# Kernel optimization log

Measured on AMD Instinct MI355X. Metric: run time of the kernel, lower is better.

The kernel has to match this reference:

```python
import jax, jax.numpy as jnp
import numpy as np

EPS_LOG = 1e-10
DECAY = 0.99
RESET_THRESHOLD = 2


def setup_inputs() -> dict:
    key = jax.random.key(0)
    ks = jax.random.split(key, 8)
    B, C_in, T = 4, 1024, 2048
    K, D = 8192, 256
    N = B * T
    return {
        "z": jax.random.normal(ks[0], (B, C_in, T), dtype=jnp.float32),
        "u": jax.random.uniform(ks[1], (N, K), dtype=jnp.float32),
        "Wi": jax.random.normal(ks[2], (D, C_in), dtype=jnp.float32) * 0.02,
        "bi": jax.random.normal(ks[3], (D,), dtype=jnp.float32) * 0.02,
        "Wo": jax.random.normal(ks[4], (C_in, D), dtype=jnp.float32) * 0.02,
        "bo": jax.random.normal(ks[5], (C_in,), dtype=jnp.float32) * 0.02,
        "embedding": jax.random.normal(ks[6], (K, D), dtype=jnp.float32),
        "cluster_size": jnp.zeros((K,), dtype=jnp.float32),
    }


def reference(z, u, Wi, bi, Wo, bo, embedding, cluster_size):
    B, _, T = z.shape
    K, D = embedding.shape
    N = B * T

    # inproj: Conv1d with kernel_size=1 == pointwise linear over channel dim
    z_e = jnp.einsum('bit,di->bdt', z, Wi) + bi[None, :, None]  # (B, D, T)
    z_d = z_e.transpose(0, 2, 1).reshape(N, D)                   # (b t) d

    # squared-euclidean distances via norm expansion
    dist = ((z_d ** 2).sum(axis=1, keepdims=True)
            - 2.0 * (z_d @ embedding.T)
            + (embedding ** 2).sum(axis=1))                      # (N, K)

    # gumbel noise (training=True), softmax_temp = 1.0
    gumbel = -jnp.log(-jnp.log(u + EPS_LOG) + EPS_LOG)
    logits = -dist + gumbel
    y_soft = jax.nn.softmax(logits, axis=-1)                     # (N, K)

    z_q_flat = y_soft @ embedding                                # (N, D)

    # kl_div(log(avg+eps), uniform target of shape (N,K), reduction='sum')
    avg_probs = y_soft.mean(axis=0)                              # (K,)
    inv_k = 1.0 / K
    kl_loss = N * jnp.sum(inv_k * (jnp.log(inv_k) - jnp.log(avg_probs + EPS_LOG)))

    indices = jnp.argmax(y_soft, axis=1)                         # (N,) int

    z_q = z_q_flat.reshape(B, T, D).transpose(0, 2, 1)           # (B, D, T)
    vq_loss = jnp.mean((z_e - jax.lax.stop_gradient(z_q)) ** 2)

    # outproj: Conv1d kernel_size=1
    out = jnp.einsum('bdt,od->bot', z_q, Wo) + bo[None, :, None]  # (B, C_in, T)

    # box_result: active_num uses cluster_size BEFORE the EMA update
    active_num = (cluster_size > RESET_THRESHOLD).sum().astype(z.dtype)
    counts = jnp.zeros((K,), z.dtype).at[indices].add(1.0)       # one-hot column sums
    probs = counts / N                                           # == mean(one_hot, axis=0)
    perplexity = jnp.exp(-jnp.sum(probs * jnp.log(probs + EPS_LOG)))
    new_cluster_size = cluster_size * DECAY + counts * (1.0 - DECAY)

    return out, vq_loss, kl_loss, perplexity, active_num, new_cluster_size
```

## Files before the change

kernel.cpp:

```cpp
#include <hip/hip_runtime.h>
#include <hip/hip_fp16.h>


#define NROWS 8192
#define KCL   8192
#define DDIM  256
#define CIN   1024
#define TSEQ  2048
#define EPSL  1e-10f
#define MHAT  (-140.0f)

#define OUT_SC   (4*CIN*TSEQ)

#define ZD_OFF   0
#define ZQ_OFF   (NROWS*DDIM)
#define E2_OFF   (2*NROWS*DDIM)
#define CS_OFF   (E2_OFF + KCL)
#define CNT_OFF  (CS_OFF + KCL)
#define VQ_OFF   (CNT_OFF + KCL)
#define LINV_OFF (VQ_OFF + 4)

#define ZD2W   0
#define ZQ2W   2097152
#define EBW    4194304
#define ETW    5242880
#define WOBW   6291456
#define ZDBW   6422528
#define E2W    7471104
#define C2W    7479296
#define LINVW  7487488
#define CSUMW  7495680
#define CNTW   7503872
#define VQW    7512064
#define PW     7512128
#define ENDW   (PW + 33554432)
#define LSPW   ZQ2W
#define CVW    (ZQ2W + 131072)
#define CIW    (ZQ2W + 393216)

using short8v = __attribute__((ext_vector_type(8))) short;
using short4v = __attribute__((ext_vector_type(4))) short;
using f32x16  = __attribute__((ext_vector_type(16))) float;

__device__ __forceinline__ ushort f2bf(float f) {
  unsigned int x = __float_as_uint(f);
  return (ushort)((x + 0x7FFFu + ((x >> 16) & 1u)) >> 16);
}
__device__ __forceinline__ float bf2f(ushort h) {
  return __uint_as_float(((unsigned int)h) << 16);
}
__device__ __forceinline__ short8v pack8(float4 a, float4 b) {
  short8v v;
  v[0] = (short)f2bf(a.x); v[1] = (short)f2bf(a.y);
  v[2] = (short)f2bf(a.z); v[3] = (short)f2bf(a.w);
  v[4] = (short)f2bf(b.x); v[5] = (short)f2bf(b.y);
  v[6] = (short)f2bf(b.z); v[7] = (short)f2bf(b.w);
  return v;
}
__device__ __forceinline__ void gload16(const void* g, void* l) {
  __builtin_amdgcn_global_load_lds(
      (const __attribute__((address_space(1))) unsigned int*)g,
      (__attribute__((address_space(3))) unsigned int*)l, 16, 0, 0);
}


__global__ __launch_bounds__(256) void e2_kernel(const float* __restrict__ E,
                                                 float* __restrict__ e2) {
  const int tid = threadIdx.x;
  const int k = blockIdx.x * 64 + (tid >> 2);
  const int p = tid & 3;
  const float* row = E + (size_t)k * DDIM + p * 64;
  float s = 0.f;
#pragma unroll
  for (int j = 0; j < 16; ++j) {
    const float4 v = *reinterpret_cast<const float4*>(row + j * 4);
    s += v.x * v.x + v.y * v.y + v.z * v.z + v.w * v.w;
  }
  s += __shfl_xor(s, 1);
  s += __shfl_xor(s, 2);
  if (p == 0) e2[k] = s;
}

__global__ __launch_bounds__(256) void e2c2_kernel(const float* __restrict__ E,
                                                   float* __restrict__ e2,
                                                   float* __restrict__ c2) {
  const int tid = threadIdx.x;
  const int k = blockIdx.x * 64 + (tid >> 2);
  const int p = tid & 3;
  const float* row = E + (size_t)k * DDIM + p * 64;
  float s = 0.f;
#pragma unroll
  for (int j = 0; j < 16; ++j) {
    const float4 v = *reinterpret_cast<const float4*>(row + j * 4);
    s += v.x * v.x + v.y * v.y + v.z * v.z + v.w * v.w;
  }
  s += __shfl_xor(s, 1);
  s += __shfl_xor(s, 2);
  if (p == 0) { e2[k] = s; c2[k] = -s - MHAT; }
}

__global__ __launch_bounds__(256) void cvtwob_kernel(const float* __restrict__ W,
                                                     ushort* __restrict__ Wb) {
  const size_t i = ((size_t)blockIdx.x * 256 + threadIdx.x) * 8;
  const float4 a = *reinterpret_cast<const float4*>(W + i);
  const float4 b = *reinterpret_cast<const float4*>(W + i + 4);
  *reinterpret_cast<short8v*>(Wb + i) = pack8(a, b);
}

__global__ __launch_bounds__(256) void etprep_kernel(const float* __restrict__ E,
                                                     ushort* __restrict__ ET,
                                                     ushort* __restrict__ EB) {
  __shared__ float tb[64 * 68];
  const int t = threadIdx.x;
  const int kb = (blockIdx.x & 127) * 64;
  const int db = (blockIdx.x >> 7) * 64;
#pragma unroll
  for (int it = 0; it < 4; ++it) {
    const int r = (t >> 4) + it * 16;
    const int c = (t & 15) * 4;
    const float4 v = *reinterpret_cast<const float4*>(E + (size_t)(kb + r) * DDIM + db + c);
    tb[r * 68 + c] = v.x; tb[r * 68 + c + 1] = v.y;
    tb[r * 68 + c + 2] = v.z; tb[r * 68 + c + 3] = v.w;
    short4v o;
    o[0] = (short)f2bf(v.x); o[1] = (short)f2bf(v.y);
    o[2] = (short)f2bf(v.z); o[3] = (short)f2bf(v.w);
    *reinterpret_cast<short4v*>(EB + (size_t)(kb + r) * DDIM + db + c) = o;
  }
  __syncthreads();
  const int dl = t >> 2, kg = (t & 3) * 16;
  short8v o0, o1;
#pragma unroll
  for (int j = 0; j < 8; ++j) o0[j] = (short)f2bf(tb[(kg + j) * 68 + dl]);
#pragma unroll
  for (int j = 0; j < 8; ++j) o1[j] = (short)f2bf(tb[(kg + 8 + j) * 68 + dl]);
  ushort* dst = ET + (size_t)(db + dl) * KCL + kb + kg;
  *reinterpret_cast<short8v*>(dst) = o0;
  *reinterpret_cast<short8v*>(dst + 8) = o1;
}

__global__ __launch_bounds__(256) void inproj32_kernel(const float* __restrict__ z,
                                                       const float* __restrict__ Wi,
                                                       const float* __restrict__ bi,
                                                       float* __restrict__ zd) {
  __shared__ float wi_s[32 * 260];
  __shared__ float zc[32 * 32];
  const int tid = threadIdx.x;
  const int nb = blockIdx.x >> 1, cih = blockIdx.x & 1;
  const int n0 = nb * 32;
  const int b = n0 / TSEQ;
  const int t0 = n0 % TSEQ;
  const float* zb = z + (size_t)b * CIN * TSEQ;
  const int ibase = cih * 512;

  const int dg = tid & 63;
  const int d0 = dg * 4;
  const int wv = tid >> 6;
  const int r0 = wv * 8;

  float acc[4][8];
#pragma unroll
  for (int c = 0; c < 4; ++c)
#pragma unroll
    for (int r = 0; r < 8; ++r) acc[c][r] = 0.f;

  for (int i0 = ibase; i0 < ibase + 512; i0 += 32) {
    __syncthreads();
    {
      const int iiq = (tid & 7) * 4;
      const int dt = tid >> 3;
#pragma unroll
      for (int p = 0; p < 8; ++p) {
        const int d = dt + p * 32;
        const float4 w = *reinterpret_cast<const float4*>(Wi + (size_t)d * CIN + i0 + iiq);
        wi_s[(iiq + 0) * 260 + d] = w.x;
        wi_s[(iiq + 1) * 260 + d] = w.y;
        wi_s[(iiq + 2) * 260 + d] = w.z;
        wi_s[(iiq + 3) * 260 + d] = w.w;
      }
      const int rr = tid & 31;
      const int iib = tid >> 5;
#pragma unroll
      for (int p = 0; p < 4; ++p) {
        const int ii = iib + p * 8;
        zc[ii * 32 + rr] = zb[(size_t)(i0 + ii) * TSEQ + t0 + rr];
      }
    }
    __syncthreads();
#pragma unroll
    for (int ii = 0; ii < 32; ++ii) {
      const float4 w = *reinterpret_cast<const float4*>(&wi_s[ii * 260 + d0]);
#pragma unroll
      for (int rq = 0; rq < 2; ++rq) {
        const float4 zv = *reinterpret_cast<const float4*>(&zc[ii * 32 + r0 + rq * 4]);
        const float zz[4] = {zv.x, zv.y, zv.z, zv.w};
#pragma unroll
        for (int q = 0; q < 4; ++q) {
          acc[0][rq * 4 + q] += w.x * zz[q];
          acc[1][rq * 4 + q] += w.y * zz[q];
          acc[2][rq * 4 + q] += w.z * zz[q];
          acc[3][rq * 4 + q] += w.w * zz[q];
        }
      }
    }
  }
  const float4 bv = *reinterpret_cast<const float4*>(bi + d0);
  const float bx = cih ? 0.f : bv.x, by = cih ? 0.f : bv.y;
  const float bz = cih ? 0.f : bv.z, bw = cih ? 0.f : bv.w;
#pragma unroll
  for (int r = 0; r < 8; ++r) {
    float* zr = zd + (size_t)(n0 + r0 + r) * DDIM + d0;
    atomicAdd(zr + 0, acc[0][r] + bx);
    atomicAdd(zr + 1, acc[1][r] + by);
    atomicAdd(zr + 2, acc[2][r] + bz);
    atomicAdd(zr + 3, acc[3][r] + bw);
  }
}

#define FSS(KT, CUR, UC, UN)                                                   \
  {                                                                            \
    const int k0 = kbase + (KT) * 32;                                          \
    __syncthreads();            \
    if ((KT) < 15) {                                                           \
      _Pragma("unroll")                                                        \
      for (int pp = 0; pp < 2; ++pp) {                                         \
        const int q = tid + pp * 512, r = q >> 5, c = q & 31;                  \
        gload16(Eb + (size_t)(k0 + 32 + r) * 256 + (size_t)(c ^ (r & 7)) * 8,  \
                &Es[(1 - (CUR)) * 8192 + q * 8]);                              \
      }                                                                        \
      const float* ubn = ubase + k0 + 32 + 4 * half;                           \
      _Pragma("unroll")                                                        \
      for (int q = 0; q < 4; ++q)                                              \
        UN[q] = *reinterpret_cast<const float4*>(ubn + q * 8);                 \
    }                                                                          \
    const ushort* Ecur = Es + (CUR) * 8192;                                    \
    f32x16 acc;                                                                \
    _Pragma("unroll")                                                          \
    for (int i = 0; i < 16; ++i) acc[i] = 0.f;                                 \
    _Pragma("unroll")                                                          \
    for (int ks = 0; ks < 16; ++ks) {                                          \
      const int cc = (ks * 2 + half) ^ (r31 & 7);                              \
      const short8v Af =                                                       \
          *reinterpret_cast<const short8v*>(Ecur + r31 * 256 + cc * 8);        \
      acc = __builtin_amdgcn_mfma_f32_32x32x16_bf16(Af, ZB[ks], acc, 0, 0, 0); \
    }                                                                          \
    ushort* pdst = P + (size_t)n * KCL + k0 + 4 * half;                        \
    _Pragma("unroll")                                                          \
    for (int q = 0; q < 4; ++q) {                                              \
      const float uu[4] = {UC[q].x, UC[q].y, UC[q].z, UC[q].w};                \
      short4v st;                                                              \
      _Pragma("unroll")                                                        \
      for (int j = 0; j < 4; ++j) {                                            \
        const int reg = q * 4 + j;                                             \
        const int kcl = k0 + q * 8 + 4 * half + j;                             \
        const float ce = c2s[kcl - kbase];                                     \
        const float D = 1e-10f - __logf(uu[j] + 1e-10f);                       \
        const float pe = __fdividef(__expf(fmaf(acc[reg], 2.f, ce)), D);       \
        psum += pe;                                                            \
        const bool cA = pe > b0v, cB = pe > b1v;                               \
        const float nv = cA ? b0v : pe; const int ni = cA ? b0i : kcl;         \
        b1v = cB ? nv : b1v; b1i = cB ? ni : b1i;                              \
        b0v = cA ? pe : b0v; b0i = cA ? kcl : b0i;                             \
        st[j] = (short)f2bf(pe);                                               \
      }                                                                        \
      *reinterpret_cast<short4v*>(pdst + q * 8) = st;                          \
    }                                                                          \
  }

__global__ __launch_bounds__(512, 2) void flashS_kernel(
    const ushort* __restrict__ ZDB, const float* __restrict__ u,
    const ushort* __restrict__ Eb, const float* __restrict__ c2,
    ushort* __restrict__ P, float* __restrict__ lsp,
    float* __restrict__ candv, int* __restrict__ candi) {
  __shared__ ushort Es[2 * 32 * 256];
  __shared__ float c2s[512];
  const int tid = threadIdx.x;
  const int l = tid & 63, w = tid >> 6;
  const int half = l >> 5;
  const int swz = (blockIdx.x & 7) * 64 + (blockIdx.x >> 3);
  const int nb = swz & 31, kq = swz >> 5;
  const int n0 = nb * 256;
  const int kbase = kq * 512;
  const int r31 = l & 31;
  const int n = n0 + w * 32 + r31;

  short8v ZB[16];
  {
    const ushort* zr = ZDB + (size_t)n * DDIM + half * 8;
#pragma unroll
    for (int ks = 0; ks < 16; ++ks)
      ZB[ks] = *reinterpret_cast<const short8v*>(zr + ks * 16);
  }

  const float* ubase = u + ((size_t)n << 13);
  c2s[tid] = c2[kbase + tid];

#pragma unroll
  for (int pp = 0; pp < 2; ++pp) {
    const int q = tid + pp * 512, r = q >> 5, c = q & 31;
    gload16(Eb + (size_t)(kbase + r) * 256 + (size_t)(c ^ (r & 7)) * 8, &Es[q * 8]);
  }
  float4 uA[4], uB[4];
  {
    const float* ub = ubase + kbase + 4 * half;
#pragma unroll
    for (int q = 0; q < 4; ++q)
      uA[q] = *reinterpret_cast<const float4*>(ub + q * 8);
  }

  float psum = 0.f;
  float b0v = -1.f, b1v = -1.f;
  int b0i = 0x7fffffff, b1i = 0x7fffffff;

  for (int kt2 = 0; kt2 < 16; kt2 += 2) {
    FSS(kt2, 0, uA, uB);
    FSS(kt2 + 1, 1, uB, uA);
  }

  psum += __shfl_xor(psum, 32);
  {
    const float ov0 = __shfl_xor(b0v, 32); const int oi0 = __shfl_xor(b0i, 32);
    const float ov1 = __shfl_xor(b1v, 32); const int oi1 = __shfl_xor(b1i, 32);
    {
      const bool cA = (ov0 > b0v) || (ov0 == b0v && oi0 < b0i);
      const bool cB = (ov0 > b1v) || (ov0 == b1v && oi0 < b1i);
      const float nv = cA ? b0v : ov0; const int ni = cA ? b0i : oi0;
      b1v = cB ? nv : b1v; b1i = cB ? ni : b1i;
      b0v = cA ? ov0 : b0v; b0i = cA ? oi0 : b0i;
    }
    {
      const bool cA = (ov1 > b0v) || (ov1 == b0v && oi1 < b0i);
      const bool cB = (ov1 > b1v) || (ov1 == b1v && oi1 < b1i);
      const float nv = cA ? b0v : ov1; const int ni = cA ? b0i : oi1;
      b1v = cB ? nv : b1v; b1i = cB ? ni : b1i;
      b0v = cA ? ov1 : b0v; b0i = cA ? oi1 : b0i;
    }
  }
  if (half == 0) {
    lsp[kq * NROWS + n] = psum;
    candv[(kq * 2 + 0) * NROWS + n] = b0v;
    candi[(kq * 2 + 0) * NROWS + n] = b0i;
    candv[(kq * 2 + 1) * NROWS + n] = b1v;
    candi[(kq * 2 + 1) * NROWS + n] = b1i;
  }
}

__global__ __launch_bounds__(256) void rowfin_kernel(
    const float* __restrict__ lsp, const float* __restrict__ candv,
    const int* __restrict__ candi, const float* __restrict__ zd,
    const float* __restrict__ E, const float* __restrict__ e2,
    const float* __restrict__ u, float* __restrict__ linv,
    float* __restrict__ counts) {
  const int l = threadIdx.x & 63;
  const int w = threadIdx.x >> 6;
  const int n = blockIdx.x * 4 + w;

  float bv[4] = {-1.f, -1.f, -1.f, -1.f};
  int bi[4] = {0x7fffffff, 0x7fffffff, 0x7fffffff, 0x7fffffff};
  if (l < 32) { bv[0] = candv[l * NROWS + n]; bi[0] = candi[l * NROWS + n]; }
#pragma unroll
  for (int mk = 1; mk < 64; mk <<= 1) {
    float ov[4]; int oi[4];
#pragma unroll
    for (int i = 0; i < 4; ++i) { ov[i] = __shfl_xor(bv[i], mk); oi[i] = __shfl_xor(bi[i], mk); }
#pragma unroll
    for (int i = 0; i < 4; ++i) {
      const float f = ov[i]; const int kk = oi[i];
      const bool c0 = (f > bv[0]) || (f == bv[0] && kk < bi[0]);
      const bool c1 = (f > bv[1]) || (f == bv[1] && kk < bi[1]);
      const bool c2 = (f > bv[2]) || (f == bv[2] && kk < bi[2]);
      const bool c3 = (f > bv[3]) || (f == bv[3] && kk < bi[3]);
      const float n3 = c2 ? bv[2] : f; const int i3 = c2 ? bi[2] : kk;
      const float n2 = c1 ? bv[1] : f; const int i2 = c1 ? bi[1] : kk;
      const float n1 = c0 ? bv[0] : f; const int i1 = c0 ? bi[0] : kk;
      bv[3] = c3 ? n3 : bv[3]; bi[3] = c3 ? i3 : bi[3];
      bv[2] = c2 ? n2 : bv[2]; bi[2] = c2 ? i2 : bi[2];
      bv[1] = c1 ? n1 : bv[1]; bi[1] = c1 ? i1 : bi[1];
      bv[0] = c0 ? f : bv[0];  bi[0] = c0 ? kk : bi[0];
    }
  }
  float ls = (l < 16) ? lsp[l * NROWS + n] : 0.f;
#pragma unroll
  for (int mk = 1; mk <= 8; mk <<= 1) ls += __shfl_xor(ls, mk);
  const float4 zv = *reinterpret_cast<const float4*>(zd + (size_t)n * DDIM + l * 4);
  float best = -1e30f; int besti = 0x7fffffff;
#pragma unroll
  for (int c = 0; c < 4; ++c) {
    const int kc = bi[c];
    const float4 ev = *reinterpret_cast<const float4*>(E + (size_t)kc * DDIM + l * 4);
    float d = zv.x * ev.x + zv.y * ev.y + zv.z * ev.z + zv.w * ev.w;
#pragma unroll
    for (int mk = 1; mk < 64; mk <<= 1) d += __shfl_xor(d, mk);
    const float uu = u[(size_t)n * KCL + kc];
    const float D = 1e-10f - __logf(uu + 1e-10f);
    const float g = -__logf(D);
    const float lg = 2.f * d - e2[kc] + g;
    if (lg > best || (lg == best && kc < besti)) { best = lg; besti = kc; }
  }
  if (l == 0) {
    atomicAdd(&counts[besti], 1.f);
    linv[n] = 1.f / ls;
  }
}

__global__ __launch_bounds__(512, 2) void pvS_kernel(
    const ushort* __restrict__ P, const ushort* __restrict__ ET,
    const float* __restrict__ linv, float* __restrict__ parts,
    float* __restrict__ colsum) {
  __shared__ ushort ps[2][64 * 64];
  __shared__ float linv_s[64];
  const int tid = threadIdx.x;
  const int l = tid & 63, w = tid >> 6;
  const int half = l >> 5;
  const int r31 = l & 31;
  const int swz = (blockIdx.x & 7) * 64 + (blockIdx.x >> 3);
  const int nb = swz & 127, ks = swz >> 7;
  const int n0 = nb * 64;
  const int kc0 = ks * 2048;
  const int nw = w & 1, dw = w >> 1;
  const int sr = tid >> 3, sc = tid & 7;

  if (tid < 64) linv_s[tid] = linv[n0 + tid];

  f32x16 acc0, acc1;
#pragma unroll
  for (int i = 0; i < 16; ++i) { acc0[i] = 0.f; acc1[i] = 0.f; }

  gload16(P + (size_t)(n0 + sr) * KCL + kc0 + (size_t)(sc ^ (sr & 7)) * 8,
          &ps[0][tid * 8]);

  for (int t = 0; t < 32; ++t) {
    const int cur = t & 1;
    const int kc = kc0 + t * 64;
    __syncthreads();
    if (t < 31) {
      gload16(P + (size_t)(n0 + sr) * KCL + kc + 64 + (size_t)(sc ^ (sr & 7)) * 8,
              &ps[1 - cur][tid * 8]);
    }
#pragma unroll
    for (int ksn = 0; ksn < 4; ++ksn) {
      const int cc = ksn * 2 + half;
      short8v a, b0, b1;
      {
        const int r = nw * 32 + r31;
        a = *reinterpret_cast<const short8v*>(&ps[cur][r * 64 + ((cc ^ (r & 7))) * 8]);
      }
      {
        const ushort* etb = ET + (size_t)(dw * 64 + r31) * KCL + kc + cc * 8;
        b0 = *reinterpret_cast<const short8v*>(etb);
        b1 = *reinterpret_cast<const short8v*>(etb + (size_t)32 * KCL);
      }
      acc0 = __builtin_amdgcn_mfma_f32_32x32x16_bf16(a, b0, acc0, 0, 0, 0);
      acc1 = __builtin_amdgcn_mfma_f32_32x32x16_bf16(a, b1, acc1, 0, 0, 0);
    }
    {
      const int c = tid >> 3;
      const int rb = tid & 7;
      float csp = 0.f;
#pragma unroll
      for (int r8 = 0; r8 < 8; ++r8) {
        const int r = rb + r8 * 8;
        const int chunk = (c >> 3) ^ (r & 7);
        csp += bf2f(ps[cur][r * 64 + chunk * 8 + (c & 7)]) * linv_s[r];
      }
      csp += __shfl_xor(csp, 1);
      csp += __shfl_xor(csp, 2);
      csp += __shfl_xor(csp, 4);
      if (rb == 0) atomicAdd(&colsum[kc + c], csp);
    }
  }
  float* pbase = parts + (size_t)ks * NROWS * DDIM;
#pragma unroll
  for (int reg = 0; reg < 16; ++reg) {
    const int dr = (reg & 3) + 8 * (reg >> 2) + 4 * half;
    float* zr = pbase + (size_t)(n0 + nw * 32 + dr) * DDIM + dw * 64 + r31;
    zr[0]  = acc0[reg];
    zr[32] = acc1[reg];
  }
}

__global__ __launch_bounds__(256) void zqred_kernel(const float* __restrict__ parts,
                                                    const float* __restrict__ linv,
                                                    const float* __restrict__ zd,
                                                    float* __restrict__ zq,
                                                    float* __restrict__ vqs) {
  const size_t i = ((size_t)blockIdx.x * 256 + threadIdx.x) * 8;
  const int n = (int)(i >> 8);
  const float lv = linv[n];
  float s = 0.f;
#pragma unroll
  for (int j = 0; j < 8; j += 4) {
    float4 p0 = *reinterpret_cast<const float4*>(parts + i + j);
    const float4 p1 = *reinterpret_cast<const float4*>(parts + i + j + (size_t)NROWS * DDIM);
    const float4 p2 = *reinterpret_cast<const float4*>(parts + i + j + (size_t)2 * NROWS * DDIM);
    const float4 p3 = *reinterpret_cast<const float4*>(parts + i + j + (size_t)3 * NROWS * DDIM);
    const float4 a = *reinterpret_cast<const float4*>(zd + i + j);
    float4 o;
    o.x = (p0.x + p1.x + p2.x + p3.x) * lv;
    o.y = (p0.y + p1.y + p2.y + p3.y) * lv;
    o.z = (p0.z + p1.z + p2.z + p3.z) * lv;
    o.w = (p0.w + p1.w + p2.w + p3.w) * lv;
    *reinterpret_cast<float4*>(zq + i + j) = o;
    const float dx = a.x - o.x, dy = a.y - o.y, dz = a.z - o.z, dw = a.w - o.w;
    s += dx * dx + dy * dy + dz * dz + dw * dw;
  }
#pragma unroll
  for (int mk = 1; mk < 64; mk <<= 1) s += __shfl_xor(s, mk);
  if ((threadIdx.x & 63) == 0) atomicAdd(vqs, s);
}

__global__ __launch_bounds__(256) void outproj2_kernel(const float* __restrict__ zq,
                                                       const ushort* __restrict__ Wob,
                                                       const float* __restrict__ bo,
                                                       float* __restrict__ outp) {
  extern __shared__ char smem[];
  ushort* zs = (ushort*)smem;
  ushort* wsld = zs + 64 * 256;
  const int tid = threadIdx.x;
  const int l = tid & 63, w = tid >> 6;
  const int half = l >> 5;
  const int nb = blockIdx.x >> 4, ob = blockIdx.x & 15;
  const int n0 = nb * 64, o0 = ob * 64;
  const int nw = w & 1, ow = w >> 1;
  {
    const int row = tid >> 2, seg = tid & 3;
    const float* zr = zq + (size_t)(n0 + row) * DDIM + seg * 64;
    const ushort* wr = Wob + (size_t)(o0 + row) * DDIM + seg * 64;
#pragma unroll
    for (int g = 0; g < 8; ++g) {
      const float4 a = *reinterpret_cast<const float4*>(zr + g * 8);
      const float4 b = *reinterpret_cast<const float4*>(zr + g * 8 + 4);
      const int c = seg * 8 + g;
      *reinterpret_cast<short8v*>(zs + row * 256 + ((c ^ (row & 7))) * 8) = pack8(a, b);
      const short8v wv = *reinterpret_cast<const short8v*>(wr + g * 8);
      *reinterpret_cast<short8v*>(wsld + row * 256 + ((c ^ (row & 7))) * 8) = wv;
    }
  }
  __syncthreads();
  f32x16 acc;
#pragma unroll
  for (int i = 0; i < 16; ++i) acc[i] = 0.f;
#pragma unroll
  for (int ksn = 0; ksn < 16; ++ksn) {
    const int cc = ksn * 2 + half;
    const int ra = nw * 32 + (l & 31);
    const int rb = ow * 32 + (l & 31);
    const short8v a = *reinterpret_cast<const short8v*>(zs + ra * 256 + ((cc ^ (ra & 7))) * 8);
    const short8v b = *reinterpret_cast<const short8v*>(wsld + rb * 256 + ((cc ^ (rb & 7))) * 8);
    acc = __builtin_amdgcn_mfma_f32_32x32x16_bf16(a, b, acc, 0, 0, 0);
  }
  const int o = o0 + ow * 32 + (l & 31);
  const float bvv = bo[o];
  const int nbase = n0 + nw * 32 + 4 * half;
#pragma unroll
  for (int rq = 0; rq < 4; ++rq) {
    const int n = nbase + rq * 8;
    const int b = n >> 11;
    const int tt = n & 2047;
    float4 ov;
    ov.x = acc[rq * 4 + 0] + bvv;
    ov.y = acc[rq * 4 + 1] + bvv;
    ov.z = acc[rq * 4 + 2] + bvv;
    ov.w = acc[rq * 4 + 3] + bvv;
    *reinterpret_cast<float4*>(outp + ((size_t)b * CIN + o) * TSEQ + tt) = ov;
  }
}

template <bool STORE_LG>
__global__ __launch_bounds__(512) void flash_kernel(
    const float* __restrict__ zd, const float* __restrict__ u,
    const float* __restrict__ E, const float* __restrict__ e2g,
    float* __restrict__ zq, float* __restrict__ colsum,
    float* __restrict__ counts, float* __restrict__ vqsum,
    float* __restrict__ linvg, __half* __restrict__ lgbuf) {
  extern __shared__ float lds[];
  float* zs = lds;
  float* es = zs + 32 * 260;
  float* e2t = es + 64 * 260;
  float* cst = e2t + 64;
  float* red = cst + 64;

  const int tid = threadIdx.x;
  const int lane = tid & 63;
  const int wv = tid >> 6;
  const int r = (lane >> 4) & 3;
  const int kg = lane & 15;
  const int row = wv * 4 + r;
  const int n0 = blockIdx.x * 32;
  const int n = n0 + row;

  {
    const int rr = tid >> 4;
    const int iq = tid & 15;
#pragma unroll
    for (int p = 0; p < 4; ++p) {
      const int i = iq * 16 + p * 4;
      *reinterpret_cast<float4*>(&zs[rr * 260 + i]) =
          *reinterpret_cast<const float4*>(zd + (size_t)(n0 + rr) * DDIM + i);
    }
  }

  float4 accp[4];
#pragma unroll
  for (int s = 0; s < 4; ++s) accp[s] = make_float4(0.f, 0.f, 0.f, 0.f);
  float lsum = 0.f;
  float best = -1e30f;
  int bidx = 0;

  const float* zrow = zs + row * 260;

  for (int t = 0; t < KCL / 64; ++t) {
    const int k0 = t * 64;
    __syncthreads();
    {
      const int iq = tid & 15;
#pragma unroll
      for (int pp = 0; pp < 2; ++pp) {
        const int kk = (tid >> 4) + pp * 32;
#pragma unroll
        for (int p = 0; p < 4; ++p) {
          const int i = iq * 16 + p * 4;
          *reinterpret_cast<float4*>(&es[kk * 260 + i]) =
              *reinterpret_cast<const float4*>(E + (size_t)(k0 + kk) * DDIM + i);
        }
      }
      if (tid < 64) e2t[tid] = e2g[k0 + tid];
    }
    __syncthreads();

    float acc4[4] = {0.f, 0.f, 0.f, 0.f};
#pragma unroll 4
    for (int i = 0; i < DDIM; i += 4) {
      const float4 zv = *reinterpret_cast<const float4*>(zrow + i);
#pragma unroll
      for (int jj = 0; jj < 4; ++jj) {
        const float4 ev = *reinterpret_cast<const float4*>(&es[(kg + jj * 16) * 260 + i]);
        acc4[jj] += zv.x * ev.x + zv.y * ev.y + zv.z * ev.z + zv.w * ev.w;
      }
    }

    float p4[4];
    float tmax = -1e30f;
    int tidx = 0;
#pragma unroll
    for (int jj = 0; jj < 4; ++jj) {
      const int kk = kg + jj * 16;
      const float uu = u[(size_t)n * KCL + k0 + kk];
      const float g = -__logf(-__logf(uu + EPSL) + EPSL);
      const float lt = 2.f * acc4[jj] - e2t[kk] + g - MHAT;
      const float pe = __expf(lt);
      p4[jj] = pe;
      lsum += pe;
      if (lt > tmax) { tmax = lt; tidx = k0 + kk; }
    }
#pragma unroll
    for (int mk = 1; mk <= 8; mk <<= 1) {
      const float ov = __shfl_xor(tmax, mk);
      const int oi = __shfl_xor(tidx, mk);
      if (ov > tmax || (ov == tmax && oi < tidx)) { tmax = ov; tidx = oi; }
    }
    if (tmax > best) { best = tmax; bidx = tidx; }

#pragma unroll
    for (int jj = 0; jj < 4; ++jj) {
#pragma unroll 4
      for (int q = 0; q < 16; ++q) {
        const int kk = jj * 16 + q;
        const float yv = __shfl(p4[jj], (lane & 48) | q);
        const float* erow = &es[kk * 260 + kg * 16];
#pragma unroll
        for (int s = 0; s < 4; ++s) {
          const int c = (s + kg) & 3;
          const float4 ev = *reinterpret_cast<const float4*>(erow + c * 4);
          accp[s].x += yv * ev.x;
          accp[s].y += yv * ev.y;
          accp[s].z += yv * ev.z;
          accp[s].w += yv * ev.w;
        }
      }
    }
  }

#pragma unroll
  for (int mk = 1; mk <= 8; mk <<= 1) lsum += __shfl_xor(lsum, mk);
  const float linv = 1.0f / lsum;

  if (kg == 0) {
    atomicAdd(&counts[bidx], 1.0f);
    linvg[n] = linv;
  }

  float vqp = 0.f;
#pragma unroll
  for (int s = 0; s < 4; ++s) {
    const int c = (s + kg) & 3;
    const int d = kg * 16 + c * 4;
    float4 o;
    o.x = accp[s].x * linv;
    o.y = accp[s].y * linv;
    o.z = accp[s].z * linv;
    o.w = accp[s].w * linv;
    *reinterpret_cast<float4*>(zq + (size_t)n * DDIM + d) = o;
    const float4 zv = *reinterpret_cast<const float4*>(zrow + d);
    const float dx = zv.x - o.x, dy = zv.y - o.y, dz = zv.z - o.z, dw = zv.w - o.w;
    vqp += dx * dx + dy * dy + dz * dz + dw * dw;
  }
#pragma unroll
  for (int mk = 1; mk <= 32; mk <<= 1) vqp += __shfl_xor(vqp, mk);
  if (lane == 0) red[wv] = vqp;
  __syncthreads();
  if (tid == 0) {
    float s = 0.f;
#pragma unroll
    for (int ww = 0; ww < 8; ++ww) s += red[ww];
    atomicAdd(vqsum, s);
  }

  if (!STORE_LG) {
    if (tid < 64) cst[tid] = 0.f;
    for (int t = 0; t < KCL / 64; ++t) {
      const int k0 = t * 64;
      __syncthreads();
      {
        const int iq = tid & 15;
#pragma unroll
        for (int pp = 0; pp < 2; ++pp) {
          const int kk = (tid >> 4) + pp * 32;
#pragma unroll
          for (int p = 0; p < 4; ++p) {
            const int i = iq * 16 + p * 4;
            *reinterpret_cast<float4*>(&es[kk * 260 + i]) =
                *reinterpret_cast<const float4*>(E + (size_t)(k0 + kk) * DDIM + i);
          }
        }
        if (tid < 64) e2t[tid] = e2g[k0 + tid];
      }
      __syncthreads();
      float acc4[4] = {0.f, 0.f, 0.f, 0.f};
#pragma unroll 4
      for (int i = 0; i < DDIM; i += 4) {
        const float4 zv = *reinterpret_cast<const float4*>(zrow + i);
#pragma unroll
        for (int jj = 0; jj < 4; ++jj) {
          const float4 ev = *reinterpret_cast<const float4*>(&es[(kg + jj * 16) * 260 + i]);
          acc4[jj] += zv.x * ev.x + zv.y * ev.y + zv.z * ev.z + zv.w * ev.w;
        }
      }
      float cs4[4];
#pragma unroll
      for (int jj = 0; jj < 4; ++jj) {
        const int kk = kg + jj * 16;
        const float uu = u[(size_t)n * KCL + k0 + kk];
        const float g = -__logf(-__logf(uu + EPSL) + EPSL);
        const float lt = 2.f * acc4[jj] - e2t[kk] + g - MHAT;
        cs4[jj] = __expf(lt) * linv;
      }
#pragma unroll
      for (int mk = 16; mk <= 32; mk <<= 1)
#pragma unroll
        for (int jj = 0; jj < 4; ++jj) cs4[jj] += __shfl_xor(cs4[jj], mk);
      if (lane < 16) {
#pragma unroll
        for (int jj = 0; jj < 4; ++jj) atomicAdd(&cst[kg + jj * 16], cs4[jj]);
      }
      __syncthreads();
      if (tid < 64) {
        atomicAdd(&colsum[k0 + tid], cst[tid]);
        cst[tid] = 0.f;
      }
    }
  }
}

__global__ __launch_bounds__(256) void outproj_kernel(const float* __restrict__ zq,
                                                      const float* __restrict__ Wo,
                                                      const float* __restrict__ bo,
                                                      float* __restrict__ outp) {
  __shared__ float wo_s[32 * 260];
  __shared__ float zc[32 * 68];
  const int tid = threadIdx.x;
  const int n0 = (blockIdx.x >> 2) * 64;
  const int ot = (blockIdx.x & 3) * 256;
  const int b = n0 / TSEQ;
  const int t0 = n0 % TSEQ;

  const int og = tid & 63;
  const int o0 = og * 4;
  const int wv = tid >> 6;
  const int r0 = wv * 16;

  float acc[4][16];
#pragma unroll
  for (int c = 0; c < 4; ++c)
#pragma unroll
    for (int r = 0; r < 16; ++r) acc[c][r] = 0.f;

  for (int dd = 0; dd < DDIM; dd += 32) {
    __syncthreads();
    {
      const int ccq = (tid & 7) * 4;
      const int oq = tid >> 3;
#pragma unroll
      for (int p = 0; p < 8; ++p) {
        const int oo = oq + p * 32;
        const float4 w = *reinterpret_cast<const float4*>(Wo + (size_t)(ot + oo) * DDIM + dd + ccq);
        wo_s[(ccq + 0) * 260 + oo] = w.x;
        wo_s[(ccq + 1) * 260 + oo] = w.y;
        wo_s[(ccq + 2) * 260 + oo] = w.z;
        wo_s[(ccq + 3) * 260 + oo] = w.w;
      }
#pragma unroll
      for (int p = 0; p < 2; ++p) {
        const int rr = oq + p * 32;
        const float4 v = *reinterpret_cast<const float4*>(zq + (size_t)(n0 + rr) * DDIM + dd + ccq);
        zc[(ccq + 0) * 68 + rr] = v.x;
        zc[(ccq + 1) * 68 + rr] = v.y;
        zc[(ccq + 2) * 68 + rr] = v.z;
        zc[(ccq + 3) * 68 + rr] = v.w;
      }
    }
    __syncthreads();
#pragma unroll
    for (int cc = 0; cc < 32; ++cc) {
      const float4 w = *reinterpret_cast<const float4*>(&wo_s[cc * 260 + o0]);
#pragma unroll
      for (int rq = 0; rq < 4; ++rq) {
        const float4 zv = *reinterpret_cast<const float4*>(&zc[cc * 68 + r0 + rq * 4]);
        const float zz[4] = {zv.x, zv.y, zv.z, zv.w};
#pragma unroll
        for (int q = 0; q < 4; ++q) {
          acc[0][rq * 4 + q] += w.x * zz[q];
          acc[1][rq * 4 + q] += w.y * zz[q];
          acc[2][rq * 4 + q] += w.z * zz[q];
          acc[3][rq * 4 + q] += w.w * zz[q];
        }
      }
    }
  }
  const float4 bv = *reinterpret_cast<const float4*>(bo + ot + o0);
  float* ob = outp + (size_t)b * CIN * TSEQ + t0;
  const float bb[4] = {bv.x, bv.y, bv.z, bv.w};
#pragma unroll
  for (int c = 0; c < 4; ++c) {
#pragma unroll
    for (int rq = 0; rq < 4; ++rq) {
      float4 o;
      o.x = acc[c][rq * 4 + 0] + bb[c];
      o.y = acc[c][rq * 4 + 1] + bb[c];
      o.z = acc[c][rq * 4 + 2] + bb[c];
      o.w = acc[c][rq * 4 + 3] + bb[c];
      *reinterpret_cast<float4*>(ob + (size_t)(ot + o0 + c) * TSEQ + r0 + rq * 4) = o;
    }
  }
}

__global__ __launch_bounds__(256) void finalize_kernel(
    const float* __restrict__ colsum, const float* __restrict__ counts,
    const float* __restrict__ vqsum, const float* __restrict__ csin,
    float* __restrict__ outsc, float* __restrict__ ncs) {
  __shared__ float rS[3][4];
  const int tid = threadIdx.x;
  const int lane = tid & 63;
  const int wv = tid >> 6;
  float sLog = 0.f, sH = 0.f, sAct = 0.f;
  for (int k = tid; k < KCL; k += 256) {
    const float avg = colsum[k] * (1.0f / NROWS);
    sLog += __logf(avg + EPSL);
    const float pb = counts[k] * (1.0f / NROWS);
    sH += pb * __logf(pb + EPSL);
    sAct += (csin[k] > 2.0f) ? 1.f : 0.f;
    ncs[k] = csin[k] * 0.99f + counts[k] * 0.01f;
  }
#pragma unroll
  for (int mk = 1; mk <= 32; mk <<= 1) {
    sLog += __shfl_xor(sLog, mk);
    sH += __shfl_xor(sH, mk);
    sAct += __shfl_xor(sAct, mk);
  }
  if (lane == 0) { rS[0][wv] = sLog; rS[1][wv] = sH; rS[2][wv] = sAct; }
  __syncthreads();
  if (tid == 0) {
    float SL = 0.f, SH = 0.f, SA = 0.f;
#pragma unroll
    for (int w = 0; w < 4; ++w) { SL += rS[0][w]; SH += rS[1][w]; SA += rS[2][w]; }
    outsc[0] = vqsum[0] * (1.0f / ((float)NROWS * (float)DDIM));
    outsc[1] = (float)NROWS * __logf(1.0f / (float)KCL) - SL;
    outsc[2] = __expf(-SH);
    outsc[3] = SA;
  }
}

extern "C" void kernel_launch(void* const* d_in, const int* in_sizes, int n_in,
                              void* d_out, int out_size, void* d_ws, size_t ws_size,
                              hipStream_t stream) {
  (void)in_sizes; (void)n_in; (void)out_size;
  const float* z = (const float*)d_in[0];
  const float* u = (const float*)d_in[1];
  const float* Wi = (const float*)d_in[2];
  const float* bi = (const float*)d_in[3];
  const float* Wo = (const float*)d_in[4];
  const float* bo = (const float*)d_in[5];
  const float* E = (const float*)d_in[6];
  const float* csin = (const float*)d_in[7];
  float* outp = (float*)d_out;
  float* ws = (float*)d_ws;

  const size_t needNew = (size_t)ENDW * 4;
  if (ws_size >= needNew) {
    ushort* EB = (ushort*)(ws + EBW);
    ushort* ET = (ushort*)(ws + ETW);
    ushort* WOB = (ushort*)(ws + WOBW);
    ushort* ZDB = (ushort*)(ws + ZDBW);
    ushort* P = (ushort*)(ws + PW);

    hipMemsetAsync((void*)(ws + CSUMW), 0, (size_t)(2 * KCL + 64) * 4, stream);
    hipMemsetAsync((void*)(ws + ZD2W), 0, (size_t)NROWS * DDIM * 4, stream);

    e2c2_kernel<<<KCL / 64, 256, 0, stream>>>(E, ws + E2W, ws + C2W);
    etprep_kernel<<<512, 256, 0, stream>>>(E, ET, EB);
    cvtwob_kernel<<<128, 256, 0, stream>>>(Wo, WOB);
    inproj32_kernel<<<512, 256, 0, stream>>>(z, Wi, bi, ws + ZD2W);
    cvtwob_kernel<<<1024, 256, 0, stream>>>(ws + ZD2W, ZDB);

    flashS_kernel<<<512, 512, 0, stream>>>(ZDB, u, EB, ws + C2W, P,
                                           ws + LSPW, ws + CVW, (int*)(ws + CIW));
    rowfin_kernel<<<NROWS / 4, 256, 0, stream>>>(ws + LSPW, ws + CVW,
                                                 (const int*)(ws + CIW),
                                                 ws + ZD2W, E, ws + E2W, u,
                                                 ws + LINVW, ws + CNTW);
    pvS_kernel<<<512, 512, 0, stream>>>(P, ET, ws + LINVW, outp, ws + CSUMW);
    zqred_kernel<<<1024, 256, 0, stream>>>(outp, ws + LINVW, ws + ZD2W,
                                           ws + ZQ2W, ws + VQW);

    hipFuncSetAttribute(reinterpret_cast<const void*>(&outproj2_kernel),
                        hipFuncAttributeMaxDynamicSharedMemorySize, 65536);
    outproj2_kernel<<<2048, 256, 65536, stream>>>(ws + ZQ2W, WOB, bo, outp);
    finalize_kernel<<<1, 256, 0, stream>>>(ws + CSUMW, ws + CNTW, ws + VQW,
                                           csin, outp + OUT_SC, outp + OUT_SC + 4);
  } else {
    hipMemsetAsync((void*)(ws + CS_OFF), 0, (size_t)(2 * KCL + 1) * sizeof(float), stream);
    hipMemsetAsync((void*)(ws + ZD_OFF), 0, (size_t)NROWS * DDIM * 4, stream);
    e2_kernel<<<KCL / 64, 256, 0, stream>>>(E, ws + E2_OFF);
    inproj32_kernel<<<512, 256, 0, stream>>>(z, Wi, bi, ws + ZD_OFF);
    const int ldsB = (32 * 260 + 64 * 260 + 64 + 64 + 16) * 4;
    hipFuncSetAttribute(reinterpret_cast<const void*>(&flash_kernel<false>),
                        hipFuncAttributeMaxDynamicSharedMemorySize, ldsB);
    flash_kernel<false><<<NROWS / 32, 512, ldsB, stream>>>(
        ws + ZD_OFF, u, E, ws + E2_OFF, ws + ZQ_OFF, ws + CS_OFF, ws + CNT_OFF,
        ws + VQ_OFF, ws + LINV_OFF, (__half*)nullptr);
    outproj_kernel<<<(NROWS / 64) * 4, 256, 0, stream>>>(ws + ZQ_OFF, Wo, bo, outp);
    finalize_kernel<<<1, 256, 0, stream>>>(ws + CS_OFF, ws + CNT_OFF, ws + VQ_OFF,
                                           csin, outp + OUT_SC, outp + OUT_SC + 4);
  }
}
```

Before: 606.9 us.

## Stage P tile stores through LDS and stage ET tiles in LDS for PV GEMM

The score kernel now writes each wave's bf16 probability tile into a padded LDS buffer and then emits coalesced 16-byte row stores to global P, replacing scattered 8-byte stores. The PV kernel drops the double-buffered async P load and instead prefetches both the P tile and the ET tile into registers. It writes them into swizzled LDS each iteration and reads the MFMA operands from LDS rather than directly from global memory. This targets uncoalesced global traffic in both kernels, at the cost of more LDS use, extra LDS round trips and an additional barrier per iteration, which could reduce occupancy or overlap.

```diff
diff --git a/kernel.cpp b/kernel.cpp
--- a/kernel.cpp
+++ b/kernel.cpp
@@ -243,7 +243,7 @@
           *reinterpret_cast<const short8v*>(Ecur + r31 * 256 + cc * 8);        \
       acc = __builtin_amdgcn_mfma_f32_32x32x16_bf16(Af, ZB[ks], acc, 0, 0, 0); \
     }                                                                          \
-    ushort* pdst = P + (size_t)n * KCL + k0 + 4 * half;                        \
+    ushort* psw = Ps + w * 1280 + r31 * 40 + 4 * half;                         \
     _Pragma("unroll")                                                          \
     for (int q = 0; q < 4; ++q) {                                              \
       const float uu[4] = {UC[q].x, UC[q].y, UC[q].z, UC[q].w};                \
@@ -262,16 +262,27 @@
         b0v = cA ? pe : b0v; b0i = cA ? kcl : b0i;                             \
         st[j] = (short)f2bf(pe);                                               \
       }                                                                        \
-      *reinterpret_cast<short4v*>(pdst + q * 8) = st;                          \
+      *reinterpret_cast<short4v*>(psw + q * 8) = st;                           \
     }                                                                          \
-  }
-
-__global__ __launch_bounds__(512, 2) void flashS_kernel(
+    asm volatile("s_waitcnt lgkmcnt(0)" ::: "memory");                         \
+    __builtin_amdgcn_sched_barrier(0);                                         \
+    {                                                                          \
+      const int frow = l >> 1, fpart = l & 1;                                  \
+      const ushort* src = Ps + w * 1280 + frow * 40 + fpart * 16;              \
+      ushort* dst = P + (size_t)(n0 + w * 32 + frow) * KCL + k0 + fpart * 16;  \
+      *reinterpret_cast<short8v*>(dst) = *reinterpret_cast<const short8v*>(src);\
+      *reinterpret_cast<short8v*>(dst + 8) =                                   \
+          *reinterpret_cast<const short8v*>(src + 8);                          \
+    }                                                                          \
+  }
+
+__global__ __launch_bounds__(512, 2) void flashS2_kernel(
     const ushort* __restrict__ ZDB, const float* __restrict__ u,
     const ushort* __restrict__ Eb, const float* __restrict__ c2,
     ushort* __restrict__ P, float* __restrict__ lsp,
     float* __restrict__ candv, int* __restrict__ candi) {
   __shared__ ushort Es[2 * 32 * 256];
+  __shared__ ushort Ps[8 * 32 * 40];
   __shared__ float c2s[512];
   const int tid = threadIdx.x;
   const int l = tid & 63, w = tid >> 6;
@@ -402,11 +413,12 @@
   }
 }
 
-__global__ __launch_bounds__(512, 2) void pvS_kernel(
+__global__ __launch_bounds__(512, 2) void pv2_kernel(
     const ushort* __restrict__ P, const ushort* __restrict__ ET,
     const float* __restrict__ linv, float* __restrict__ parts,
     float* __restrict__ colsum) {
-  __shared__ ushort ps[2][64 * 64];
+  __shared__ ushort ps[64 * 64];
+  __shared__ ushort es[256 * 64];
   __shared__ float linv_s[64];
   const int tid = threadIdx.x;
   const int l = tid & 63, w = tid >> 6;
@@ -417,7 +429,6 @@
   const int n0 = nb * 64;
   const int kc0 = ks * 2048;
   const int nw = w & 1, dw = w >> 1;
-  const int sr = tid >> 3, sc = tid & 7;
 
   if (tid < 64) linv_s[tid] = linv[n0 + tid];
 
@@ -425,30 +436,46 @@
 #pragma unroll
   for (int i = 0; i < 16; ++i) { acc0[i] = 0.f; acc1[i] = 0.f; }
 
-  gload16(P + (size_t)(n0 + sr) * KCL + kc0 + (size_t)(sc ^ (sr & 7)) * 8,
-          &ps[0][tid * 8]);
-
+  short8v rp, re[4];
+  {
+    const int r = tid >> 3, c = tid & 7;
+    rp = *reinterpret_cast<const short8v*>(P + (size_t)(n0 + r) * KCL + kc0 + c * 8);
+#pragma unroll
+    for (int pp = 0; pp < 4; ++pp) {
+      const int q = tid * 4 + pp; const int rr = q >> 3, cc = q & 7;
+      re[pp] = *reinterpret_cast<const short8v*>(ET + (size_t)rr * KCL + kc0 + cc * 8);
+    }
+  }
   for (int t = 0; t < 32; ++t) {
-    const int cur = t & 1;
-    const int kc = kc0 + t * 64;
+    {
+      const int r = tid >> 3, c = tid & 7;
+      *reinterpret_cast<short8v*>(ps + r * 64 + ((c ^ (r & 7))) * 8) = rp;
+    }
+#pragma unroll
+    for (int pp = 0; pp < 4; ++pp) {
+      const int q = tid * 4 + pp; const int rr = q >> 3, cc = q & 7;
+      *reinterpret_cast<short8v*>(es + rr * 64 + ((cc ^ (rr & 7))) * 8) = re[pp];
+    }
     __syncthreads();
     if (t < 31) {
-      gload16(P + (size_t)(n0 + sr) * KCL + kc + 64 + (size_t)(sc ^ (sr & 7)) * 8,
-              &ps[1 - cur][tid * 8]);
+      const int kc = kc0 + (t + 1) * 64;
+      {
+        const int r = tid >> 3, c = tid & 7;
+        rp = *reinterpret_cast<const short8v*>(P + (size_t)(n0 + r) * KCL + kc + c * 8);
+      }
+#pragma unroll
+      for (int pp = 0; pp < 4; ++pp) {
+        const int q = tid * 4 + pp; const int rr = q >> 3, cc = q & 7;
+        re[pp] = *reinterpret_cast<const short8v*>(ET + (size_t)rr * KCL + kc + cc * 8);
+      }
     }
 #pragma unroll
     for (int ksn = 0; ksn < 4; ++ksn) {
       const int cc = ksn * 2 + half;
       short8v a, b0, b1;
-      {
-        const int r = nw * 32 + r31;
-        a = *reinterpret_cast<const short8v*>(&ps[cur][r * 64 + ((cc ^ (r & 7))) * 8]);
-      }
-      {
-        const ushort* etb = ET + (size_t)(dw * 64 + r31) * KCL + kc + cc * 8;
-        b0 = *reinterpret_cast<const short8v*>(etb);
-        b1 = *reinterpret_cast<const short8v*>(etb + (size_t)32 * KCL);
-      }
+      { const int r = nw * 32 + r31;      a  = *reinterpret_cast<const short8v*>(ps + r * 64 + ((cc ^ (r & 7))) * 8); }
+      { const int r = dw * 64 + r31;      b0 = *reinterpret_cast<const short8v*>(es + r * 64 + ((cc ^ (r & 7))) * 8); }
+      { const int r = dw * 64 + 32 + r31; b1 = *reinterpret_cast<const short8v*>(es + r * 64 + ((cc ^ (r & 7))) * 8); }
       acc0 = __builtin_amdgcn_mfma_f32_32x32x16_bf16(a, b0, acc0, 0, 0, 0);
       acc1 = __builtin_amdgcn_mfma_f32_32x32x16_bf16(a, b1, acc1, 0, 0, 0);
     }
@@ -460,13 +487,14 @@
       for (int r8 = 0; r8 < 8; ++r8) {
         const int r = rb + r8 * 8;
         const int chunk = (c >> 3) ^ (r & 7);
-        csp += bf2f(ps[cur][r * 64 + chunk * 8 + (c & 7)]) * linv_s[r];
+        csp += bf2f(ps[r * 64 + chunk * 8 + (c & 7)]) * linv_s[r];
       }
       csp += __shfl_xor(csp, 1);
       csp += __shfl_xor(csp, 2);
       csp += __shfl_xor(csp, 4);
-      if (rb == 0) atomicAdd(&colsum[kc + c], csp);
-    }
+      if (rb == 0) atomicAdd(&colsum[kc0 + t * 64 + c], csp);
+    }
+    __syncthreads();
   }
   float* pbase = parts + (size_t)ks * NROWS * DDIM;
 #pragma unroll
@@ -921,13 +949,13 @@
     inproj32_kernel<<<512, 256, 0, stream>>>(z, Wi, bi, ws + ZD2W);
     cvtwob_kernel<<<1024, 256, 0, stream>>>(ws + ZD2W, ZDB);
 
-    flashS_kernel<<<512, 512, 0, stream>>>(ZDB, u, EB, ws + C2W, P,
-                                           ws + LSPW, ws + CVW, (int*)(ws + CIW));
+    flashS2_kernel<<<512, 512, 0, stream>>>(ZDB, u, EB, ws + C2W, P,
+                                            ws + LSPW, ws + CVW, (int*)(ws + CIW));
     rowfin_kernel<<<NROWS / 4, 256, 0, stream>>>(ws + LSPW, ws + CVW,
                                                  (const int*)(ws + CIW),
                                                  ws + ZD2W, E, ws + E2W, u,
                                                  ws + LINVW, ws + CNTW);
-    pvS_kernel<<<512, 512, 0, stream>>>(P, ET, ws + LINVW, outp, ws + CSUMW);
+    pv2_kernel<<<512, 512, 0, stream>>>(P, ET, ws + LINVW, outp, ws + CSUMW);
     zqred_kernel<<<1024, 256, 0, stream>>>(outp, ws + LINVW, ws + ZD2W,
                                            ws + ZQ2W, ws + VQW);
 
```

Result: faster. 489.2 us (-19.4%).
